# Kernel optimization log

Measured on AMD Instinct MI355X. Metric: run time of the kernel, lower is better.

Reference implementation:

```python
import jax, jax.numpy as jnp
import numpy as np
import math

WIDTH = 1024
NUM_HEADS = 16
HEAD_DIM = WIDTH // NUM_HEADS
WINDOW_SIZE = 256
MIN_LOGITS_VALUE = -1e30


def setup_inputs() -> dict:
    key = jax.random.key(0)
    ks = jax.random.split(key, 7)
    b, t = 2, 2048
    std = math.sqrt(1.0 / WIDTH)
    x = jax.random.normal(ks[0], (b, t, WIDTH), dtype=jnp.float32)
    segment_pos = jnp.broadcast_to(jnp.arange(t, dtype=jnp.int32)[None, :], (b, t))
    Wq = jax.random.normal(ks[1], (WIDTH, WIDTH), dtype=jnp.float32) * std
    Wk = jax.random.normal(ks[2], (HEAD_DIM, WIDTH), dtype=jnp.float32) * std
    Wv = jax.random.normal(ks[3], (HEAD_DIM, WIDTH), dtype=jnp.float32) * std
    Wf = jax.random.normal(ks[4], (WIDTH, WIDTH), dtype=jnp.float32) * std
    bf = jnp.zeros((WIDTH,), dtype=jnp.float32)
    return {"x": x, "segment_pos": segment_pos, "Wq": Wq, "Wk": Wk, "Wv": Wv, "Wf": Wf, "bf": bf}


def reference(x, segment_pos, Wq, Wk, Wv, Wf, bf):
    b, t, _ = x.shape
    # projections (Linear: x @ W.T)
    q = (x @ Wq.T).reshape(b, t, NUM_HEADS, HEAD_DIM)  # [b,t,n,h]
    k = x @ Wk.T  # [b,t,h] single shared KV head (MQA)
    v = x @ Wv.T  # [b,t,h]
    scale = 1.0 / math.sqrt(HEAD_DIM)
    logits = jnp.einsum('btnh,bsh->bnts', q, k) * scale  # [b,n,t,s]
    # sliding-window causal mask: q_pos >= k_pos and q_pos <= k_pos + window
    ar = jnp.arange(t)
    qp = ar[:, None]
    kp = ar[None, :]
    mask = (qp >= kp) & (qp <= kp + WINDOW_SIZE)  # [t,s]
    masked = jnp.where(mask[None, None, :, :], logits, MIN_LOGITS_VALUE)
    probs = jax.nn.softmax(masked.astype(jnp.float32), axis=-1).astype(logits.dtype)
    out = jnp.einsum('bnts,bsh->btnh', probs, v)  # [b,t,n,h]
    out = out.reshape(b, t, WIDTH)
    return out @ Wf.T + bf
```

## Files before the change

kernel.cpp:

```cpp
#include <hip/hip_runtime.h>
#include <stdint.h>

#define B_SZ   2
#define T_SEQ  2048
#define WIDTH_ 1024
#define NH     16
#define HD     64
#define WIN    256
#define MROWS  (B_SZ * T_SEQ)
#define NQKV   1152

typedef __attribute__((ext_vector_type(4))) float f32x4;
typedef __attribute__((ext_vector_type(8))) short s16x8;

typedef __attribute__((address_space(1))) const void gas_void;
typedef __attribute__((address_space(3))) void las_void;

#define MFMA(a, b, c) __builtin_amdgcn_mfma_f32_16x16x32_bf16((a), (b), (c), 0, 0, 0)

#define VM_WAIT4() asm volatile("s_waitcnt vmcnt(4)" ::: "memory")
#define VM_WAIT0() asm volatile("s_waitcnt vmcnt(0)" ::: "memory")

__device__ __forceinline__ void gload_lds16(const void* g, void* l) {
  __builtin_amdgcn_global_load_lds((gas_void*)g, (las_void*)l, 16, 0, 0);
}

__device__ __forceinline__ ushort f2bf(float f) {
  union { float f; uint32_t u; } v; v.f = f;
  uint32_t u = v.u;
  return (ushort)((u + 0x7FFFu + ((u >> 16) & 1u)) >> 16);
}

__global__ void prep_kernel(const float* __restrict__ x,
                            const float* __restrict__ Wq,
                            const float* __restrict__ Wk,
                            const float* __restrict__ Wv,
                            const float* __restrict__ Wf,
                            ushort* __restrict__ xb,
                            ushort* __restrict__ wqkv,
                            ushort* __restrict__ wfb) {
  const int XN = MROWS * WIDTH_ / 4;
  const int WQ = NQKV * WIDTH_ / 4;
  const int WF = WIDTH_ * WIDTH_ / 4;
  int i = blockIdx.x * blockDim.x + threadIdx.x;
  float4 v;
  ushort* dst;
  if (i < XN) {
    v = ((const float4*)x)[i];
    dst = xb + i * 4;
  } else if (i < XN + WQ) {
    int j = i - XN;
    int row = (j * 4) >> 10;
    int col = (j * 4) & 1023;
    const float* src = (row < 1024) ? (Wq + row * 1024 + col)
                     : (row < 1088) ? (Wk + (row - 1024) * 1024 + col)
                                    : (Wv + (row - 1088) * 1024 + col);
    v = *(const float4*)src;
    dst = wqkv + j * 4;
  } else if (i < XN + WQ + WF) {
    int j = i - XN - WQ;
    v = ((const float4*)Wf)[j];
    dst = wfb + j * 4;
  } else {
    return;
  }
  ushort4 o;
  o.x = f2bf(v.x); o.y = f2bf(v.y); o.z = f2bf(v.z); o.w = f2bf(v.w);
  *(ushort4*)dst = o;
}

#define G_STAGE64(AS, BS, KOFF) do {                                        \
  _Pragma("unroll")                                                         \
  for (int i_ = 0; i_ < 2; ++i_) {                                          \
    int c_ = i_ * 256 + w * 64 + lane;                          \
    int row_ = c_ >> 3;                         \
    int ke_ = ((c_ & 7) * 8) ^ ((row_ & 7) << 3);      \
    int ldsb_ = (i_ * 256 + w * 64) * 16;            \
    gload_lds16(A + (size_t)(m0 + row_) * 1024 + (KOFF) + ke_,              \
                (char*)(AS) + ldsb_);                                       \
    gload_lds16(B + (size_t)(n0 + row_) * 1024 + (KOFF) + ke_,              \
                (char*)(BS) + ldsb_);                                       \
  }                                                                         \
} while (0)

#define G_COMPUTE64(AS, BS) do {                                            \
  _Pragma("unroll")                                                         \
  for (int ks_ = 0; ks_ < 2; ++ks_) {                                       \
    s16x8 af_[2], bf_[2];                                                   \
    _Pragma("unroll")                                                       \
    for (int t_ = 0; t_ < 2; ++t_) {                                        \
      int ra_ = wm + t_ * 16 + r16;                                         \
      int rb_ = wn + t_ * 16 + r16;                                         \
      af_[t_] = *(const s16x8*)&(AS)[ra_ * 64 +                             \
                  ((ks_ * 32 + g * 8) ^ ((ra_ & 7) << 3))];                 \
      bf_[t_] = *(const s16x8*)&(BS)[rb_ * 64 +                             \
                  ((ks_ * 32 + g * 8) ^ ((rb_ & 7) << 3))];                 \
    }                                                                       \
    _Pragma("unroll")                                                       \
    for (int mb_ = 0; mb_ < 2; ++mb_)                                       \
      _Pragma("unroll")                                                     \
      for (int nb_ = 0; nb_ < 2; ++nb_)                                     \
        acc[mb_][nb_] = MFMA(af_[mb_], bf_[nb_], acc[mb_][nb_]);            \
  }                                                                         \
} while (0)

#define G_ITER(AS, BS, K)  do {                                             \
  if ((K) == 960) { VM_WAIT0(); } else { VM_WAIT4(); }                      \
  __syncthreads();                                                          \
  G_COMPUTE64(AS, BS);                                                      \
  __syncthreads();                                                          \
  if ((K) + 128 < 1024) G_STAGE64(AS, BS, (K) + 128);                       \
} while (0)

template <int MODE>
__global__ __launch_bounds__(256) void gemm_kernel(
    const ushort* __restrict__ A, const ushort* __restrict__ B,
    ushort* __restrict__ qb, ushort* __restrict__ kb, ushort* __restrict__ vt,
    float* __restrict__ Cf, const float* __restrict__ bias) {
  const int NBX = (MODE == 0) ? 18 : 16;
  const int nwg = NBX * 64;
  const int cpx = nwg >> 3;
  int swz = (blockIdx.x & 7) * cpx + (blockIdx.x >> 3);
  const int bx = swz % NBX;
  const int by = swz / NBX;

  const int w = threadIdx.x >> 6;
  const int lane = threadIdx.x & 63;
  const int g = lane >> 4;
  const int r16 = lane & 15;
  const int m0 = by * 64;
  const int n0 = bx * 64;
  const int wm = (w >> 1) * 32;
  const int wn = (w & 1) * 32;

  __shared__ ushort As0[64 * 64];
  __shared__ ushort Bs0[64 * 64];
  __shared__ ushort As1[64 * 64];
  __shared__ ushort Bs1[64 * 64];

  f32x4 acc[2][2] = {};

  G_STAGE64(As0, Bs0, 0);
  G_STAGE64(As1, Bs1, 64);
#pragma unroll
  for (int k0 = 0; k0 < 1024; k0 += 128) {
    G_ITER(As0, Bs0, k0);
    G_ITER(As1, Bs1, k0 + 64);
  }

#pragma unroll
  for (int mb = 0; mb < 2; ++mb)
#pragma unroll
    for (int nb = 0; nb < 2; ++nb) {
      int n = n0 + wn + nb * 16 + r16;
      int mbase = m0 + wm + mb * 16 + 4 * g;
      if (MODE == 0) {
#pragma unroll
        for (int r = 0; r < 4; ++r) {
          ushort h = f2bf(acc[mb][nb][r]);
          int m = mbase + r;
          if (n < 1024)      qb[m * 1024 + n] = h;
          else if (n < 1088) kb[m * 64 + (n - 1024)] = h;
          else               vt[((size_t)((m >> 11) * 64 + (n - 1088))) * 2048 +
                                (m & 2047)] = h;
        }
      } else {
        float bv = bias[n];
#pragma unroll
        for (int r = 0; r < 4; ++r)
          Cf[(size_t)(mbase + r) * 1024 + n] = acc[mb][nb][r] + bv;
      }
    }
}

__global__ __launch_bounds__(64, 2) void attn_kernel(
    const ushort* __restrict__ qb, const ushort* __restrict__ kb,
    const ushort* __restrict__ vt, ushort* __restrict__ ao) {
  const int lane = threadIdx.x;
  const int g = lane >> 4;
  const int r16 = lane & 15;
  const int blk = blockIdx.x;
  const int qt = blk & 63;
  const int h = (blk >> 6) & 15;
  const int b = blk >> 10;
  const int q0 = qt * 32;
  const int qpA = q0 + r16;
  const int qpB = q0 + 16 + r16;

  const ushort* qrowA = qb + (size_t)(b * 2048 + qpA) * 1024 + h * 64;
  const ushort* qrowB = qb + (size_t)(b * 2048 + qpB) * 1024 + h * 64;
  s16x8 qfA0 = *(const s16x8*)(qrowA + g * 8);
  s16x8 qfA1 = *(const s16x8*)(qrowA + 32 + g * 8);
  s16x8 qfB0 = *(const s16x8*)(qrowB + g * 8);
  s16x8 qfB1 = *(const s16x8*)(qrowB + 32 + g * 8);

  f32x4 oaccA[4] = {}, oaccB[4] = {};
  float mA = -1e30f, lA = 0.f, mB = -1e30f, lB = 0.f;

  int kt0 = q0 - WIN;
  if (kt0 < 0) kt0 = 0;
  kt0 &= ~31;

  s16x8 pk[4][2];
#pragma unroll
  for (int s = 0; s < 4; ++s) {
    const ushort* kp = kb + (size_t)(b * 2048 + kt0 + s * 16 + r16) * 64;
    pk[s][0] = *(const s16x8*)(kp + g * 8);
    pk[s][1] = *(const s16x8*)(kp + 32 + g * 8);
  }

  for (int kt = kt0; kt <= q0; kt += 64) {
    s16x8 c[4][2];
#pragma unroll
    for (int s = 0; s < 4; ++s) { c[s][0] = pk[s][0]; c[s][1] = pk[s][1]; }

    s16x8 vfr[4][2];
#pragma unroll
    for (int db = 0; db < 4; ++db) {
      const ushort* vrow = vt + (size_t)(b * 64 + db * 16 + r16) * 2048 + kt;
      uint2 va0 = *(const uint2*)(vrow + 4 * g);
      uint2 va1 = *(const uint2*)(vrow + 16 + 4 * g);
      uint2 vb0 = *(const uint2*)(vrow + 32 + 4 * g);
      uint2 vb1 = *(const uint2*)(vrow + 48 + 4 * g);
      union { s16x8 v; uint32_t d[4]; } u0, u1;
      u0.d[0] = va0.x; u0.d[1] = va0.y; u0.d[2] = va1.x; u0.d[3] = va1.y;
      u1.d[0] = vb0.x; u1.d[1] = vb0.y; u1.d[2] = vb1.x; u1.d[3] = vb1.y;
      vfr[db][0] = u0.v; vfr[db][1] = u1.v;
    }

    if (kt + 64 <= q0) {
#pragma unroll
      for (int s = 0; s < 4; ++s) {
        const ushort* kp = kb + (size_t)(b * 2048 + kt + 64 + s * 16 + r16) * 64;
        pk[s][0] = *(const s16x8*)(kp + g * 8);
        pk[s][1] = *(const s16x8*)(kp + 32 + g * 8);
      }
    }

    f32x4 sA[4], sB[4];
    __builtin_amdgcn_s_setprio(1);
#pragma unroll
    for (int s = 0; s < 4; ++s) {
      f32x4 z = {};
      sA[s] = MFMA(c[s][0], qfA0, z); sA[s] = MFMA(c[s][1], qfA1, sA[s]);
      sB[s] = MFMA(c[s][0], qfB0, z); sB[s] = MFMA(c[s][1], qfB1, sB[s]);
    }
    __builtin_amdgcn_s_setprio(0);

    float pA[4][4], pB[4][4];
    float tmA = -1e30f, tmB = -1e30f;
#pragma unroll
    for (int s = 0; s < 4; ++s)
#pragma unroll
      for (int r = 0; r < 4; ++r) {
        int ka = kt + s * 16 + 4 * g + r;
        float a = (ka <= qpA && qpA - ka <= WIN) ? sA[s][r] * 0.125f : -1e30f;
        float bv = (ka <= qpB && qpB - ka <= WIN) ? sB[s][r] * 0.125f : -1e30f;
        pA[s][r] = a; pB[s][r] = bv;
        tmA = fmaxf(tmA, a); tmB = fmaxf(tmB, bv);
      }
    tmA = fmaxf(tmA, __shfl_xor(tmA, 16));
    tmA = fmaxf(tmA, __shfl_xor(tmA, 32));
    tmB = fmaxf(tmB, __shfl_xor(tmB, 16));
    tmB = fmaxf(tmB, __shfl_xor(tmB, 32));

    float mnA = fmaxf(mA, tmA), mnB = fmaxf(mB, tmB);
    float corrA = __expf(mA - mnA), corrB = __expf(mB - mnB);
    float tsA = 0.f, tsB = 0.f;
    s16x8 pfA0, pfA1, pfB0, pfB1;
#pragma unroll
    for (int r = 0; r < 4; ++r) {
      float eA0 = __expf(pA[0][r] - mnA);
      float eA1 = __expf(pA[1][r] - mnA);
      float eA2 = __expf(pA[2][r] - mnA);
      float eA3 = __expf(pA[3][r] - mnA);
      float eB0 = __expf(pB[0][r] - mnB);
      float eB1 = __expf(pB[1][r] - mnB);
      float eB2 = __expf(pB[2][r] - mnB);
      float eB3 = __expf(pB[3][r] - mnB);
      tsA += (eA0 + eA1) + (eA2 + eA3);
      tsB += (eB0 + eB1) + (eB2 + eB3);
      pfA0[r] = (short)f2bf(eA0); pfA0[4 + r] = (short)f2bf(eA1);
      pfA1[r] = (short)f2bf(eA2); pfA1[4 + r] = (short)f2bf(eA3);
      pfB0[r] = (short)f2bf(eB0); pfB0[4 + r] = (short)f2bf(eB1);
      pfB1[r] = (short)f2bf(eB2); pfB1[4 + r] = (short)f2bf(eB3);
    }
    tsA += __shfl_xor(tsA, 16); tsA += __shfl_xor(tsA, 32);
    tsB += __shfl_xor(tsB, 16); tsB += __shfl_xor(tsB, 32);
    lA = lA * corrA + tsA; mA = mnA;
    lB = lB * corrB + tsB; mB = mnB;

#pragma unroll
    for (int db = 0; db < 4; ++db) { oaccA[db] *= corrA; oaccB[db] *= corrB; }

    __builtin_amdgcn_s_setprio(1);
#pragma unroll
    for (int db = 0; db < 4; ++db) {
      oaccA[db] = MFMA(vfr[db][0], pfA0, oaccA[db]);
      oaccA[db] = MFMA(vfr[db][1], pfA1, oaccA[db]);
      oaccB[db] = MFMA(vfr[db][0], pfB0, oaccB[db]);
      oaccB[db] = MFMA(vfr[db][1], pfB1, oaccB[db]);
    }
    __builtin_amdgcn_s_setprio(0);
  }

  float invA = 1.0f / lA, invB = 1.0f / lB;
  ushort* orowA = ao + (size_t)(b * 2048 + qpA) * 1024 + h * 64;
  ushort* orowB = ao + (size_t)(b * 2048 + qpB) * 1024 + h * 64;
#pragma unroll
  for (int db = 0; db < 4; ++db) {
    ushort4 oA, oB;
    oA.x = f2bf(oaccA[db][0] * invA); oA.y = f2bf(oaccA[db][1] * invA);
    oA.z = f2bf(oaccA[db][2] * invA); oA.w = f2bf(oaccA[db][3] * invA);
    oB.x = f2bf(oaccB[db][0] * invB); oB.y = f2bf(oaccB[db][1] * invB);
    oB.z = f2bf(oaccB[db][2] * invB); oB.w = f2bf(oaccB[db][3] * invB);
    *(ushort4*)(orowA + db * 16 + 4 * g) = oA;
    *(ushort4*)(orowB + db * 16 + 4 * g) = oB;
  }
}

extern "C" void kernel_launch(void* const* d_in, const int* in_sizes, int n_in,
                              void* d_out, int out_size, void* d_ws, size_t ws_size,
                              hipStream_t stream) {
  const float* x  = (const float*)d_in[0];
  const float* Wq = (const float*)d_in[2];
  const float* Wk = (const float*)d_in[3];
  const float* Wv = (const float*)d_in[4];
  const float* Wf = (const float*)d_in[5];
  const float* bf = (const float*)d_in[6];
  float* out = (float*)d_out;

  uint8_t* w8 = (uint8_t*)d_ws;
  ushort* xb   = (ushort*)(w8 + 0);
  ushort* qbuf = (ushort*)(w8 + 8388608);
  ushort* attn = (ushort*)(w8 + 16777216);
  ushort* wqkv = (ushort*)(w8 + 25165824);
  ushort* wfb  = (ushort*)(w8 + 27525120);
  ushort* kbuf = (ushort*)(w8 + 29622272);
  ushort* vt   = (ushort*)(w8 + 30146560);

  prep_kernel<<<6272, 256, 0, stream>>>(x, Wq, Wk, Wv, Wf, xb, wqkv, wfb);
  gemm_kernel<0><<<1152, 256, 0, stream>>>(xb, wqkv, qbuf, kbuf, vt,
                                           nullptr, nullptr);
  attn_kernel<<<2048, 64, 0, stream>>>(qbuf, kbuf, vt, attn);
  gemm_kernel<1><<<1024, 256, 0, stream>>>(attn, wfb, nullptr, nullptr,
                                           nullptr, out, bf);
}
```

Before: 152.9 us.

## Use 128x128 split-K GEMM tiles with combine kernels and fixed-offset softmax

Both GEMMs move from 64x64 tiles to 128x128 tiles with a 2-way split over K, each split writing fp32 partials to workspace. New combine kernels sum the partials and apply the bf16/Q/K/Vt scatter or the bias. The LDS layout drops the XOR swizzle, so bank conflicts are possible. Attention replaces the online max-tracking softmax with exp(s*scale - 8) and a final sum, which removes reductions and rescaling but can overflow or underflow for inputs outside the expected range.

```diff
diff --git a/kernel.cpp b/kernel.cpp
--- a/kernel.cpp
+++ b/kernel.cpp
@@ -17,9 +17,7 @@
 typedef __attribute__((address_space(3))) void las_void;
 
 #define MFMA(a, b, c) __builtin_amdgcn_mfma_f32_16x16x32_bf16((a), (b), (c), 0, 0, 0)
-
-#define VM_WAIT4() asm volatile("s_waitcnt vmcnt(4)" ::: "memory")
-#define VM_WAIT0() asm volatile("s_waitcnt vmcnt(0)" ::: "memory")
+#define VMEM_DRAIN() asm volatile("s_waitcnt vmcnt(0)" ::: "memory")
 
 __device__ __forceinline__ void gload_lds16(const void* g, void* l) {
   __builtin_amdgcn_global_load_lds((gas_void*)g, (las_void*)l, 16, 0, 0);
@@ -69,12 +67,12 @@
   *(ushort4*)dst = o;
 }
 
-#define G_STAGE64(AS, BS, KOFF) do {                                        \
+#define G_STAGE(AS, BS, KOFF) do {                                          \
   _Pragma("unroll")                                                         \
   for (int i_ = 0; i_ < 2; ++i_) {                                          \
     int c_ = i_ * 256 + w * 64 + lane;                          \
-    int row_ = c_ >> 3;                         \
-    int ke_ = ((c_ & 7) * 8) ^ ((row_ & 7) << 3);      \
+    int row_ = c_ >> 2;                                                     \
+    int ke_ = (c_ & 3) * 8;                                                 \
     int ldsb_ = (i_ * 256 + w * 64) * 16;            \
     gload_lds16(A + (size_t)(m0 + row_) * 1024 + (KOFF) + ke_,              \
                 (char*)(AS) + ldsb_);                                       \
@@ -83,94 +81,115 @@
   }                                                                         \
 } while (0)
 
-#define G_COMPUTE64(AS, BS) do {                                            \
+#define G_COMPUTE(AS, BS) do {                                              \
+  s16x8 af_[4], bf_[4];                                                     \
   _Pragma("unroll")                                                         \
-  for (int ks_ = 0; ks_ < 2; ++ks_) {                                       \
-    s16x8 af_[2], bf_[2];                                                   \
+  for (int t_ = 0; t_ < 4; ++t_) {                                          \
+    af_[t_] = *(const s16x8*)&(AS)[(wm + t_ * 16 + r16) * 32 + g * 8];      \
+    bf_[t_] = *(const s16x8*)&(BS)[(wn + t_ * 16 + r16) * 32 + g * 8];      \
+  }                                                                         \
+  _Pragma("unroll")                                                         \
+  for (int mb_ = 0; mb_ < 4; ++mb_)                                         \
     _Pragma("unroll")                                                       \
-    for (int t_ = 0; t_ < 2; ++t_) {                                        \
-      int ra_ = wm + t_ * 16 + r16;                                         \
-      int rb_ = wn + t_ * 16 + r16;                                         \
-      af_[t_] = *(const s16x8*)&(AS)[ra_ * 64 +                             \
-                  ((ks_ * 32 + g * 8) ^ ((ra_ & 7) << 3))];                 \
-      bf_[t_] = *(const s16x8*)&(BS)[rb_ * 64 +                             \
-                  ((ks_ * 32 + g * 8) ^ ((rb_ & 7) << 3))];                 \
-    }                                                                       \
-    _Pragma("unroll")                                                       \
-    for (int mb_ = 0; mb_ < 2; ++mb_)                                       \
-      _Pragma("unroll")                                                     \
-      for (int nb_ = 0; nb_ < 2; ++nb_)                                     \
-        acc[mb_][nb_] = MFMA(af_[mb_], bf_[nb_], acc[mb_][nb_]);            \
-  }                                                                         \
-} while (0)
-
-#define G_ITER(AS, BS, K)  do {                                             \
-  if ((K) == 960) { VM_WAIT0(); } else { VM_WAIT4(); }                      \
-  __syncthreads();                                                          \
-  G_COMPUTE64(AS, BS);                                                      \
-  __syncthreads();                                                          \
-  if ((K) + 128 < 1024) G_STAGE64(AS, BS, (K) + 128);                       \
+    for (int nb_ = 0; nb_ < 4; ++nb_)                                       \
+      acc[mb_][nb_] = MFMA(af_[mb_], bf_[nb_], acc[mb_][nb_]);              \
 } while (0)
 
 template <int MODE>
 __global__ __launch_bounds__(256) void gemm_kernel(
     const ushort* __restrict__ A, const ushort* __restrict__ B,
-    ushort* __restrict__ qb, ushort* __restrict__ kb, ushort* __restrict__ vt,
-    float* __restrict__ Cf, const float* __restrict__ bias) {
-  const int NBX = (MODE == 0) ? 18 : 16;
-  const int nwg = NBX * 64;
+    float* __restrict__ part) {
+  const int NBX = (MODE == 0) ? 9 : 8;
+  const int N   = (MODE == 0) ? 1152 : 1024;
+  const int nwg = NBX * 32 * 2;
   const int cpx = nwg >> 3;
-  int swz = (blockIdx.x & 7) * cpx + (blockIdx.x >> 3);
-  const int bx = swz % NBX;
-  const int by = swz / NBX;
+  int swz = ((int)blockIdx.x & 7) * cpx + ((int)blockIdx.x >> 3);
+  const int half = nwg >> 1;
+  const int bz = swz / half;
+  const int rem = swz % half;
+  const int bx = rem % NBX;
+  const int by = rem / NBX;
 
   const int w = threadIdx.x >> 6;
   const int lane = threadIdx.x & 63;
   const int g = lane >> 4;
   const int r16 = lane & 15;
-  const int m0 = by * 64;
-  const int n0 = bx * 64;
-  const int wm = (w >> 1) * 32;
-  const int wn = (w & 1) * 32;
-
-  __shared__ ushort As0[64 * 64];
-  __shared__ ushort Bs0[64 * 64];
-  __shared__ ushort As1[64 * 64];
-  __shared__ ushort Bs1[64 * 64];
-
-  f32x4 acc[2][2] = {};
-
-  G_STAGE64(As0, Bs0, 0);
-  G_STAGE64(As1, Bs1, 64);
-#pragma unroll
-  for (int k0 = 0; k0 < 1024; k0 += 128) {
-    G_ITER(As0, Bs0, k0);
-    G_ITER(As1, Bs1, k0 + 64);
-  }
-
-#pragma unroll
-  for (int mb = 0; mb < 2; ++mb)
-#pragma unroll
-    for (int nb = 0; nb < 2; ++nb) {
+  const int m0 = by * 128;
+  const int n0 = bx * 128;
+  const int wm = (w >> 1) * 64;
+  const int wn = (w & 1) * 64;
+  const int kb0 = bz * 512;
+
+  __shared__ ushort As0[128 * 32];
+  __shared__ ushort Bs0[128 * 32];
+  __shared__ ushort As1[128 * 32];
+  __shared__ ushort Bs1[128 * 32];
+
+  f32x4 acc[4][4] = {};
+
+  G_STAGE(As0, Bs0, kb0);
+  for (int k0 = kb0; k0 < kb0 + 512; k0 += 64) {
+    VMEM_DRAIN();
+    __syncthreads();
+    G_STAGE(As1, Bs1, k0 + 32);
+    G_COMPUTE(As0, Bs0);
+    VMEM_DRAIN();
+    __syncthreads();
+    if (k0 + 64 < kb0 + 512) G_STAGE(As0, Bs0, k0 + 64);
+    G_COMPUTE(As1, Bs1);
+  }
+
+  float* P = part + (size_t)bz * MROWS * N;
+#pragma unroll
+  for (int mb = 0; mb < 4; ++mb)
+#pragma unroll
+    for (int nb = 0; nb < 4; ++nb) {
       int n = n0 + wn + nb * 16 + r16;
       int mbase = m0 + wm + mb * 16 + 4 * g;
-      if (MODE == 0) {
-#pragma unroll
-        for (int r = 0; r < 4; ++r) {
-          ushort h = f2bf(acc[mb][nb][r]);
-          int m = mbase + r;
-          if (n < 1024)      qb[m * 1024 + n] = h;
-          else if (n < 1088) kb[m * 64 + (n - 1024)] = h;
-          else               vt[((size_t)((m >> 11) * 64 + (n - 1088))) * 2048 +
-                                (m & 2047)] = h;
-        }
-      } else {
-        float bv = bias[n];
-#pragma unroll
-        for (int r = 0; r < 4; ++r)
-          Cf[(size_t)(mbase + r) * 1024 + n] = acc[mb][nb][r] + bv;
-      }
-    }
+#pragma unroll
+      for (int r = 0; r < 4; ++r)
+        P[(size_t)(mbase + r) * N + n] = acc[mb][nb][r];
+    }
+}
+
+__global__ void combine0_kernel(const float* __restrict__ part,
+                                ushort* __restrict__ qb,
+                                ushort* __restrict__ kb,
+                                ushort* __restrict__ vt) {
+  int id = blockIdx.x * blockDim.x + threadIdx.x;
+  int m = id / 288;
+  int n0 = (id % 288) * 4;
+  const float* p0 = part + (size_t)m * 1152 + n0;
+  const float* p1 = p0 + (size_t)MROWS * 1152;
+  float s0 = p0[0] + p1[0], s1 = p0[1] + p1[1];
+  float s2 = p0[2] + p1[2], s3 = p0[3] + p1[3];
+  ushort4 o;
+  o.x = f2bf(s0); o.y = f2bf(s1); o.z = f2bf(s2); o.w = f2bf(s3);
+  if (n0 < 1024) {
+    *(ushort4*)&qb[(size_t)m * 1024 + n0] = o;
+  } else if (n0 < 1088) {
+    *(ushort4*)&kb[(size_t)m * 64 + (n0 - 1024)] = o;
+  } else {
+    int bb = m >> 11, t = m & 2047, d = n0 - 1088;
+    vt[((size_t)(bb * 64 + d + 0)) * 2048 + t] = o.x;
+    vt[((size_t)(bb * 64 + d + 1)) * 2048 + t] = o.y;
+    vt[((size_t)(bb * 64 + d + 2)) * 2048 + t] = o.z;
+    vt[((size_t)(bb * 64 + d + 3)) * 2048 + t] = o.w;
+  }
+}
+
+__global__ void combine1_kernel(const float* __restrict__ part,
+                                const float* __restrict__ bias,
+                                float* __restrict__ out) {
+  int id = blockIdx.x * blockDim.x + threadIdx.x;
+  int n0 = (id & 255) * 4;
+  const float4 a = *(const float4*)(part + (size_t)id * 4);
+  const float4 b = *(const float4*)(part + (size_t)MROWS * 1024 + (size_t)id * 4);
+  const float4 bv = *(const float4*)(bias + n0);
+  float4 o;
+  o.x = a.x + b.x + bv.x; o.y = a.y + b.y + bv.y;
+  o.z = a.z + b.z + bv.z; o.w = a.w + b.w + bv.w;
+  *(float4*)(out + (size_t)id * 4) = o;
 }
 
 __global__ __launch_bounds__(64, 2) void attn_kernel(
@@ -195,7 +214,7 @@
   s16x8 qfB1 = *(const s16x8*)(qrowB + 32 + g * 8);
 
   f32x4 oaccA[4] = {}, oaccB[4] = {};
-  float mA = -1e30f, lA = 0.f, mB = -1e30f, lB = 0.f;
+  float lA = 0.f, lB = 0.f;
 
   int kt0 = q0 - WIN;
   if (kt0 < 0) kt0 = 0;
@@ -247,51 +266,24 @@
     }
     __builtin_amdgcn_s_setprio(0);
 
-    float pA[4][4], pB[4][4];
-    float tmA = -1e30f, tmB = -1e30f;
-#pragma unroll
-    for (int s = 0; s < 4; ++s)
-#pragma unroll
-      for (int r = 0; r < 4; ++r) {
-        int ka = kt + s * 16 + 4 * g + r;
-        float a = (ka <= qpA && qpA - ka <= WIN) ? sA[s][r] * 0.125f : -1e30f;
-        float bv = (ka <= qpB && qpB - ka <= WIN) ? sB[s][r] * 0.125f : -1e30f;
-        pA[s][r] = a; pB[s][r] = bv;
-        tmA = fmaxf(tmA, a); tmB = fmaxf(tmB, bv);
+    s16x8 pfA0, pfA1, pfB0, pfB1;
+#pragma unroll
+    for (int r = 0; r < 4; ++r) {
+      int ka0 = kt + 4 * g + r;
+#pragma unroll
+      for (int s = 0; s < 4; ++s) {
+        int ka = ka0 + s * 16;
+        float eA = (ka <= qpA && qpA - ka <= WIN)
+                     ? __expf(sA[s][r] * 0.125f - 8.f) : 0.f;
+        float eB = (ka <= qpB && qpB - ka <= WIN)
+                     ? __expf(sB[s][r] * 0.125f - 8.f) : 0.f;
+        lA += eA; lB += eB;
+        if (s < 2) { pfA0[s * 4 + r] = (short)f2bf(eA);
+                     pfB0[s * 4 + r] = (short)f2bf(eB); }
+        else       { pfA1[(s - 2) * 4 + r] = (short)f2bf(eA);
+                     pfB1[(s - 2) * 4 + r] = (short)f2bf(eB); }
       }
-    tmA = fmaxf(tmA, __shfl_xor(tmA, 16));
-    tmA = fmaxf(tmA, __shfl_xor(tmA, 32));
-    tmB = fmaxf(tmB, __shfl_xor(tmB, 16));
-    tmB = fmaxf(tmB, __shfl_xor(tmB, 32));
-
-    float mnA = fmaxf(mA, tmA), mnB = fmaxf(mB, tmB);
-    float corrA = __expf(mA - mnA), corrB = __expf(mB - mnB);
-    float tsA = 0.f, tsB = 0.f;
-    s16x8 pfA0, pfA1, pfB0, pfB1;
-#pragma unroll
-    for (int r = 0; r < 4; ++r) {
-      float eA0 = __expf(pA[0][r] - mnA);
-      float eA1 = __expf(pA[1][r] - mnA);
-      float eA2 = __expf(pA[2][r] - mnA);
-      float eA3 = __expf(pA[3][r] - mnA);
-      float eB0 = __expf(pB[0][r] - mnB);
-      float eB1 = __expf(pB[1][r] - mnB);
-      float eB2 = __expf(pB[2][r] - mnB);
-      float eB3 = __expf(pB[3][r] - mnB);
-      tsA += (eA0 + eA1) + (eA2 + eA3);
-      tsB += (eB0 + eB1) + (eB2 + eB3);
-      pfA0[r] = (short)f2bf(eA0); pfA0[4 + r] = (short)f2bf(eA1);
-      pfA1[r] = (short)f2bf(eA2); pfA1[4 + r] = (short)f2bf(eA3);
-      pfB0[r] = (short)f2bf(eB0); pfB0[4 + r] = (short)f2bf(eB1);
-      pfB1[r] = (short)f2bf(eB2); pfB1[4 + r] = (short)f2bf(eB3);
-    }
-    tsA += __shfl_xor(tsA, 16); tsA += __shfl_xor(tsA, 32);
-    tsB += __shfl_xor(tsB, 16); tsB += __shfl_xor(tsB, 32);
-    lA = lA * corrA + tsA; mA = mnA;
-    lB = lB * corrB + tsB; mB = mnB;
-
-#pragma unroll
-    for (int db = 0; db < 4; ++db) { oaccA[db] *= corrA; oaccB[db] *= corrB; }
+    }
 
     __builtin_amdgcn_s_setprio(1);
 #pragma unroll
@@ -303,6 +295,9 @@
     }
     __builtin_amdgcn_s_setprio(0);
   }
+
+  lA += __shfl_xor(lA, 16); lA += __shfl_xor(lA, 32);
+  lB += __shfl_xor(lB, 16); lB += __shfl_xor(lB, 32);
 
   float invA = 1.0f / lA, invB = 1.0f / lB;
   ushort* orowA = ao + (size_t)(b * 2048 + qpA) * 1024 + h * 64;
@@ -331,18 +326,20 @@
   float* out = (float*)d_out;
 
   uint8_t* w8 = (uint8_t*)d_ws;
-  ushort* xb   = (ushort*)(w8 + 0);
-  ushort* qbuf = (ushort*)(w8 + 8388608);
-  ushort* attn = (ushort*)(w8 + 16777216);
-  ushort* wqkv = (ushort*)(w8 + 25165824);
-  ushort* wfb  = (ushort*)(w8 + 27525120);
-  ushort* kbuf = (ushort*)(w8 + 29622272);
-  ushort* vt   = (ushort*)(w8 + 30146560);
+  ushort* xb    = (ushort*)(w8 + 0);
+  ushort* wqkv  = (ushort*)(w8 + 8388608);
+  ushort* wfb   = (ushort*)(w8 + 10747904);
+  ushort* qbuf  = (ushort*)(w8 + 12845056);
+  ushort* attn  = (ushort*)(w8 + 21233664);
+  ushort* kbuf  = (ushort*)(w8 + 29622272);
+  ushort* vt    = (ushort*)(w8 + 30146560);
+  float*  part0 = (float*)(w8 + 30670848);
+  float*  part1 = (float*)(w8 + 68419584);
 
   prep_kernel<<<6272, 256, 0, stream>>>(x, Wq, Wk, Wv, Wf, xb, wqkv, wfb);
-  gemm_kernel<0><<<1152, 256, 0, stream>>>(xb, wqkv, qbuf, kbuf, vt,
-                                           nullptr, nullptr);
+  gemm_kernel<0><<<576, 256, 0, stream>>>(xb, wqkv, part0);
+  combine0_kernel<<<4608, 256, 0, stream>>>(part0, qbuf, kbuf, vt);
   attn_kernel<<<2048, 64, 0, stream>>>(qbuf, kbuf, vt, attn);
-  gemm_kernel<1><<<1024, 256, 0, stream>>>(attn, wfb, nullptr, nullptr,
-                                           nullptr, out, bf);
-}
+  gemm_kernel<1><<<512, 256, 0, stream>>>(attn, wfb, part1);
+  combine1_kernel<<<4096, 256, 0, stream>>>(part1, bf, out);
+}
```

Measured after the change: 164.8 us. 7.8% more time.
